# Optimization experiments

Hardware: AMD Instinct MI355X
Metric: run time of the kernel (lower is better)

## Reference

```python
import jax, jax.numpy as jnp
import numpy as np

B, S, H, R = 4, 4096, 768, 242
HK = H // 3  # k/v/attn-output feature dim (256)
THETA = 10000.0


def _rope_table(seq_len, dim, theta=THETA):
    # Reproduces LlamaRotaryEmbedding.forward: returns [seq_len, dim] = cat(sin, cos)
    pos = jnp.arange(seq_len, dtype=jnp.float32)
    freqs = theta ** (-jnp.arange(0, dim, 2, dtype=jnp.float32) / dim)  # [dim/2]
    ang = pos[:, None] * freqs[None, :]  # [S, dim/2]
    return jnp.concatenate([jnp.sin(ang), jnp.cos(ang)], axis=-1)  # [S, dim]


def setup_inputs() -> dict:
    key = jax.random.key(0)
    ks = jax.random.split(key, 9)
    init = lambda k, shape: (jax.random.normal(k, shape, dtype=jnp.float32) * 0.02)
    return {
        "x": jax.random.normal(ks[0], (B, S, H), dtype=jnp.float32),
        # torch nn.Linear weights have shape [out_features, in_features]; y = x @ W.T
        "q_low": init(ks[1], (R, H)),  "q_high": init(ks[2], (H, R)),
        "k_low": init(ks[3], (R, H)),  "k_high": init(ks[4], (HK, R)),
        "v_low": init(ks[5], (R, H)),  "v_high": init(ks[6], (HK, R)),
        "o_low": init(ks[7], (R, HK)), "o_high": init(ks[8], (H, R)),
    }


def reference(x, q_low, q_high, k_low, k_high, v_low, v_high, o_low, o_high):
    b, s, h = x.shape
    # NOTE: in the original module, rope_emb(q) / rope_emb(k) discard the projected
    # q/k values and return the same [S, H] sin/cos position table, so q_proj/k_proj
    # are dead code (XLA will DCE them). We keep only the live computation.
    v = (x @ v_low.T) @ v_high.T  # [B, S, HK] factorized v projection
    t = _rope_table(s, h)         # q = k = t, shape [S, H]
    attn = jax.nn.softmax(t @ t.T, axis=-1)  # [S, S], input-independent
    ctx = jnp.einsum('st,btd->bsd', attn, v)  # [B, S, HK]
    return (ctx @ o_low.T) @ o_high.T         # [B, S, H]
```

## Files before the change

kernel.cpp:

```cpp
#include <hip/hip_runtime.h>
#include <hip/hip_bf16.h>


typedef __bf16 bf16x8 __attribute__((ext_vector_type(8)));
typedef __bf16 bf16x4 __attribute__((ext_vector_type(4)));
typedef float  f32x4  __attribute__((ext_vector_type(4)));

#define GLD16(g, l) __builtin_amdgcn_global_load_lds(                         \
    (const __attribute__((address_space(1))) void*)(g),                       \
    (__attribute__((address_space(3))) void*)(l), 16, 0, 0)


__global__ __launch_bounds__(256) void prep_ptvlt(const float* __restrict__ vh,
                                                  const float* __restrict__ ol,
                                                  const float* __restrict__ vl,
                                                  __bf16* __restrict__ pt,
                                                  __bf16* __restrict__ vlt) {
    if (blockIdx.x < 242) {
        int j = blockIdx.x, i = threadIdx.x;
        float s = 0.f;
        if (i < 242) {
#pragma unroll 32
            for (int k = 0; k < 256; ++k)
                s += vh[k * 242 + i] * ol[j * 256 + k];
        }
        pt[j * 256 + i] = (__bf16)s;
    } else {
        int n = (blockIdx.x - 242) * 256 + threadIdx.x;
        int i = n >> 8, r = n & 255;
        vlt[n] = (r < 242) ? (__bf16)vl[r * 768 + i] : (__bf16)0.f;
    }
}

__global__ __launch_bounds__(256) void prep_q(const __bf16* __restrict__ pt,
                                              const float* __restrict__ oh,
                                              __bf16* __restrict__ qb) {
    int j = blockIdx.x, r = threadIdx.x;
    float s = 0.f;
#pragma unroll 32
    for (int k = 0; k < 242; ++k)
        s += (float)pt[k * 256 + r] * oh[j * 242 + k];
    qb[j * 256 + r] = (__bf16)s;
}

__global__ __launch_bounds__(256) void gemm_nt_w(const __bf16* __restrict__ A,
                                                 const __bf16* __restrict__ Bt,
                                                 __bf16* __restrict__ C) {
    __shared__ alignas(16) __bf16 lA[8 * 64 * 32];
    __shared__ alignas(16) __bf16 lB[8 * 64 * 32];

    const int tid  = threadIdx.x;
    const int wave = tid >> 6, lane = tid & 63;
    const int quad = lane >> 4, l16 = lane & 15;
    const int wm = (wave >> 1) * 32, wn = (wave & 1) * 32;

    const __bf16* Ab = A + (long)blockIdx.x * 64 * 256;
    const __bf16* Bb = Bt + (long)blockIdx.y * 64 * 256;

    const int sr = wave * 16 + (lane >> 2);
    const int sc = (lane & 3) * 8;
#pragma unroll
    for (int kc = 0; kc < 8; ++kc) {
        GLD16(Ab + sr * 256 + kc * 32 + sc, &lA[kc * 2048 + wave * 512]);
        GLD16(Bb + sr * 256 + kc * 32 + sc, &lB[kc * 2048 + wave * 512]);
    }
    __syncthreads();

    f32x4 acc[2][2] = {};
#pragma unroll
    for (int kc = 0; kc < 8; ++kc) {
        bf16x8 af[2], bfr[2];
#pragma unroll
        for (int i = 0; i < 2; ++i) {
            af[i]  = *(const bf16x8*)&lA[kc * 2048 + (wm + i * 16 + l16) * 32 + quad * 8];
            bfr[i] = *(const bf16x8*)&lB[kc * 2048 + (wn + i * 16 + l16) * 32 + quad * 8];
        }
#pragma unroll
        for (int mi = 0; mi < 2; ++mi)
#pragma unroll
            for (int ni = 0; ni < 2; ++ni)
                acc[mi][ni] = __builtin_amdgcn_mfma_f32_16x16x32_bf16(
                    af[mi], bfr[ni], acc[mi][ni], 0, 0, 0);
    }

    const int rb = blockIdx.x * 64 + wm + quad * 4;
    const int ib = blockIdx.y * 64 + wn + l16;
#pragma unroll
    for (int mi = 0; mi < 2; ++mi)
#pragma unroll
        for (int ni = 0; ni < 2; ++ni) {
            const int i  = ib + ni * 16;
            const int kc = i >> 5, qi = (i >> 3) & 3, e = i & 7;
#pragma unroll
            for (int j = 0; j < 4; ++j) {
                const int r = rb + mi * 16 + j;
                const int g = r >> 4, lr = r & 15;
                C[((g * 24 + kc) * 64 + qi * 16 + lr) * 8 + e] =
                    (__bf16)acc[mi][ni][j];
            }
        }
}

__global__ __launch_bounds__(1024, 4) void gemm_xw(const float* __restrict__ A,
                                                   const __bf16* __restrict__ Bt,
                                                   float* __restrict__ C) {
    __shared__ __bf16 lA[2][64 * 72];

    const int tid  = threadIdx.x;
    const int wave = tid >> 6, lane = tid & 63;
    const int quad = lane >> 4, l16 = lane & 15;

    const int mt = blockIdx.x;
    const float* Ab = A + (long)mt * 64 * 768;

    const int srow = tid >> 4, scol = (tid & 15) * 4;
    const float* ga = Ab + srow * 768 + scol;

    const __bf16* Bw = Bt + (long)wave * 3 * 24 * 512 + lane * 8;

    f32x4 acc[3][4] = {};
    bf16x8 bcur[3][2], bnxt[3][2];

    f32x4 a0 = *(const f32x4*)(ga);
#pragma unroll
    for (int g = 0; g < 3; ++g)
#pragma unroll
        for (int kf = 0; kf < 2; ++kf)
            bcur[g][kf] = *(const bf16x8*)(Bw + ((g * 24 + kf) << 9));
    {
        bf16x4 h = { (__bf16)a0[0], (__bf16)a0[1], (__bf16)a0[2], (__bf16)a0[3] };
        *(bf16x4*)&lA[0][srow * 72 + scol] = h;
    }
    __syncthreads();

#pragma unroll
    for (int c = 0; c < 12; ++c) {
        const int cur = c & 1, nxt = cur ^ 1;
        const int koff = (c + 1) * 64;

        if (c < 11) {
            a0 = *(const f32x4*)(ga + koff);
#pragma unroll
            for (int g = 0; g < 3; ++g)
#pragma unroll
                for (int kf = 0; kf < 2; ++kf)
                    bnxt[g][kf] = *(const bf16x8*)
                        (Bw + ((g * 24 + (c + 1) * 2 + kf) << 9));
        }

#pragma unroll
        for (int kf = 0; kf < 2; ++kf) {
            bf16x8 af[4];
#pragma unroll
            for (int m = 0; m < 4; ++m)
                af[m] = *(const bf16x8*)
                        &lA[cur][(m * 16 + l16) * 72 + kf * 32 + quad * 8];
#pragma unroll
            for (int g = 0; g < 3; ++g)
#pragma unroll
                for (int m = 0; m < 4; ++m)
                    acc[g][m] = __builtin_amdgcn_mfma_f32_16x16x32_bf16(
                        af[m], bcur[g][kf], acc[g][m], 0, 0, 0);
        }

        if (c < 11) {
            bf16x4 h = { (__bf16)a0[0], (__bf16)a0[1], (__bf16)a0[2], (__bf16)a0[3] };
            *(bf16x4*)&lA[nxt][srow * 72 + scol] = h;
#pragma unroll
            for (int g = 0; g < 3; ++g)
#pragma unroll
                for (int kf = 0; kf < 2; ++kf)
                    bcur[g][kf] = bnxt[g][kf];
            __syncthreads();
        }
    }

    const long rb = (long)mt * 64 + quad * 4;
    const int  cb = wave * 48 + l16;
#pragma unroll
    for (int g = 0; g < 3; ++g)
#pragma unroll
        for (int m = 0; m < 4; ++m)
#pragma unroll
            for (int j = 0; j < 4; ++j)
                C[(rb + m * 16 + j) * 768 + cb + g * 16] = acc[g][m][j];
}


extern "C" void kernel_launch(void* const* d_in, const int* in_sizes, int n_in,
                              void* d_out, int out_size, void* d_ws, size_t ws_size,
                              hipStream_t stream) {
    const float* x      = (const float*)d_in[0];
    const float* v_low  = (const float*)d_in[5];
    const float* v_high = (const float*)d_in[6];
    const float* o_low  = (const float*)d_in[7];
    const float* o_high = (const float*)d_in[8];
    float* out = (float*)d_out;

    char* ws = (char*)d_ws;
    __bf16* pt  = (__bf16*)(ws + 0);
    __bf16* qb  = (__bf16*)(ws + 262144);
    __bf16* vlt = (__bf16*)(ws + 655360);
    __bf16* wtb = (__bf16*)(ws + 1048576);

    prep_ptvlt<<<1010, 256, 0, stream>>>(v_high, o_low, v_low, pt, vlt);
    prep_q    <<<768,  256, 0, stream>>>(pt, o_high, qb);

    gemm_nt_w<<<dim3(12, 12), 256, 0, stream>>>(qb, vlt, wtb);

    gemm_xw<<<256, 1024, 0, stream>>>(x, wtb, out);
}
```

Measured before the change: 155.6 us.

## Use 256-wide K chunks with XOR-swizzled LDS in x·W GEMM

Restructures the gemm_xw main loop from twelve 64-wide K chunks into three 256-wide chunks. Each thread now stages 16 floats per row as bf16 into a larger double-buffered LDS tile, using an XOR swizzle instead of row padding to avoid bank conflicts. B fragments are now loaded directly inside the inner kf loop rather than prefetched one chunk ahead. The goal is fewer barriers and wider global loads; the cost is 64 KB of LDS per block, which limits occupancy, and less latency hiding for the B loads.

```diff
diff --git a/kernel.cpp b/kernel.cpp
--- a/kernel.cpp
+++ b/kernel.cpp
@@ -104,7 +104,7 @@
 __global__ __launch_bounds__(1024, 4) void gemm_xw(const float* __restrict__ A,
                                                    const __bf16* __restrict__ Bt,
                                                    float* __restrict__ C) {
-    __shared__ __bf16 lA[2][64 * 72];
+    __shared__ alignas(16) __bf16 lA[2][64 * 256];
 
     const int tid  = threadIdx.x;
     const int wave = tid >> 6, lane = tid & 63;
@@ -113,64 +113,72 @@
     const int mt = blockIdx.x;
     const float* Ab = A + (long)mt * 64 * 768;
 
-    const int srow = tid >> 4, scol = (tid & 15) * 4;
-    const float* ga = Ab + srow * 768 + scol;
+    const int srow = tid >> 4;
+    const float* ga = Ab + srow * 768 + (tid & 15) * 16;
+    const int sw  = (srow & 7) << 4;
+    const int wb0 = srow * 512 + (((tid & 15) * 32)      ^ sw);
+    const int wb1 = srow * 512 + (((tid & 15) * 32 + 16) ^ sw);
+    const int rsw = (l16 & 7) << 4;
 
     const __bf16* Bw = Bt + (long)wave * 3 * 24 * 512 + lane * 8;
 
     f32x4 acc[3][4] = {};
-    bf16x8 bcur[3][2], bnxt[3][2];
-
-    f32x4 a0 = *(const f32x4*)(ga);
-#pragma unroll
-    for (int g = 0; g < 3; ++g)
-#pragma unroll
-        for (int kf = 0; kf < 2; ++kf)
-            bcur[g][kf] = *(const bf16x8*)(Bw + ((g * 24 + kf) << 9));
+
     {
-        bf16x4 h = { (__bf16)a0[0], (__bf16)a0[1], (__bf16)a0[2], (__bf16)a0[3] };
-        *(bf16x4*)&lA[0][srow * 72 + scol] = h;
+        f32x4 s0 = *(const f32x4*)(ga);
+        f32x4 s1 = *(const f32x4*)(ga + 4);
+        f32x4 s2 = *(const f32x4*)(ga + 8);
+        f32x4 s3 = *(const f32x4*)(ga + 12);
+        bf16x8 h0 = { (__bf16)s0[0], (__bf16)s0[1], (__bf16)s0[2], (__bf16)s0[3],
+                      (__bf16)s1[0], (__bf16)s1[1], (__bf16)s1[2], (__bf16)s1[3] };
+        bf16x8 h1 = { (__bf16)s2[0], (__bf16)s2[1], (__bf16)s2[2], (__bf16)s2[3],
+                      (__bf16)s3[0], (__bf16)s3[1], (__bf16)s3[2], (__bf16)s3[3] };
+        *(bf16x8*)((char*)&lA[0][0] + wb0) = h0;
+        *(bf16x8*)((char*)&lA[0][0] + wb1) = h1;
     }
     __syncthreads();
 
 #pragma unroll
-    for (int c = 0; c < 12; ++c) {
-        const int cur = c & 1, nxt = cur ^ 1;
-        const int koff = (c + 1) * 64;
-
-        if (c < 11) {
-            a0 = *(const f32x4*)(ga + koff);
+    for (int c = 0; c < 3; ++c) {
+        f32x4 s0, s1, s2, s3;
+        if (c < 2) {
+            const float* gn = ga + (c + 1) * 256;
+            s0 = *(const f32x4*)(gn);
+            s1 = *(const f32x4*)(gn + 4);
+            s2 = *(const f32x4*)(gn + 8);
+            s3 = *(const f32x4*)(gn + 12);
+        }
+
+        const char* lb = (const char*)&lA[c & 1][0];
+#pragma unroll
+        for (int kf = 0; kf < 8; ++kf) {
+            bf16x8 b[3];
 #pragma unroll
             for (int g = 0; g < 3; ++g)
-#pragma unroll
-                for (int kf = 0; kf < 2; ++kf)
-                    bnxt[g][kf] = *(const bf16x8*)
-                        (Bw + ((g * 24 + (c + 1) * 2 + kf) << 9));
-        }
-
-#pragma unroll
-        for (int kf = 0; kf < 2; ++kf) {
+                b[g] = *(const bf16x8*)(Bw + ((g * 24 + c * 8 + kf) << 9));
             bf16x8 af[4];
 #pragma unroll
-            for (int m = 0; m < 4; ++m)
-                af[m] = *(const bf16x8*)
-                        &lA[cur][(m * 16 + l16) * 72 + kf * 32 + quad * 8];
+            for (int m = 0; m < 4; ++m) {
+                const int off = (m * 16 + l16) * 512 +
+                                ((kf * 64 + quad * 16) ^ rsw);
+                af[m] = *(const bf16x8*)(lb + off);
+            }
 #pragma unroll
             for (int g = 0; g < 3; ++g)
 #pragma unroll
                 for (int m = 0; m < 4; ++m)
                     acc[g][m] = __builtin_amdgcn_mfma_f32_16x16x32_bf16(
-                        af[m], bcur[g][kf], acc[g][m], 0, 0, 0);
-        }
-
-        if (c < 11) {
-            bf16x4 h = { (__bf16)a0[0], (__bf16)a0[1], (__bf16)a0[2], (__bf16)a0[3] };
-            *(bf16x4*)&lA[nxt][srow * 72 + scol] = h;
-#pragma unroll
-            for (int g = 0; g < 3; ++g)
-#pragma unroll
-                for (int kf = 0; kf < 2; ++kf)
-                    bcur[g][kf] = bnxt[g][kf];
+                        af[m], b[g], acc[g][m], 0, 0, 0);
+        }
+
+        if (c < 2) {
+            bf16x8 h0 = { (__bf16)s0[0], (__bf16)s0[1], (__bf16)s0[2], (__bf16)s0[3],
+                          (__bf16)s1[0], (__bf16)s1[1], (__bf16)s1[2], (__bf16)s1[3] };
+            bf16x8 h1 = { (__bf16)s2[0], (__bf16)s2[1], (__bf16)s2[2], (__bf16)s2[3],
+                          (__bf16)s3[0], (__bf16)s3[1], (__bf16)s3[2], (__bf16)s3[3] };
+            char* wp = (char*)&lA[(c + 1) & 1][0];
+            *(bf16x8*)(wp + wb0) = h0;
+            *(bf16x8*)(wp + wb1) = h1;
             __syncthreads();
         }
     }
```

After: 145.9 us. 6.2% less time.
